# Kernel optimization log

Hardware: AMD Instinct MI355X
Metric: run time of the kernel (lower is better)

## Reference

```python
import jax, jax.numpy as jnp
import numpy as np

DIM, NH, HD = 1536, 12, 128
H, W, NFPB = 22, 40, 3
S = H * W * NFPB            # 2640 query tokens
PAST = 12 * H * W           # 10560 cached kv tokens
MAXF = 150                  # rope cache frames
EPS = 1e-6


def rmsnorm(y, g):
    # torch nn.RMSNorm over last dim
    return y * jax.lax.rsqrt(jnp.mean(y * y, axis=-1, keepdims=True) + EPS) * g


def build_rope_cache(freqs):
    # freqs: [MAXF, HD//2] angles -> flat (t,h,w) grid cache [MAXF*H*W, HD]
    hd2 = HD // 2               # 64
    c_h = hd2 // 3              # 21
    c_w = hd2 // 3              # 21
    c_t = hd2 - c_h - c_w       # 22
    f_t = freqs[:MAXF, :c_t]                       # [150, 22]
    f_h = freqs[:H, c_t:c_t + c_h]                 # [22, 21]
    f_w = freqs[:W, c_t + c_h:]                    # [40, 21]
    t_grid = jnp.broadcast_to(f_t[:, None, None, :], (MAXF, H, W, c_t))
    h_grid = jnp.broadcast_to(f_h[None, :, None, :], (MAXF, H, W, c_h))
    w_grid = jnp.broadcast_to(f_w[None, None, :, :], (MAXF, H, W, c_w))
    flat = jnp.concatenate([t_grid, h_grid, w_grid], -1).reshape(-1, hd2)
    return jnp.cos(flat), jnp.sin(flat)            # each [MAXF*H*W, 64]


def apply_rope_interleaved(t, cos, sin):
    # t: [s, n, HD]; cos/sin: [s, HD//2]; is_neox=False -> interleaved pairs
    te = t[..., 0::2]
    to = t[..., 1::2]
    c = cos[:, None, :]
    s = sin[:, None, :]
    oe = te * c - to * s
    oo = to * c + te * s
    return jnp.stack([oe, oo], axis=-1).reshape(t.shape)


def setup_inputs() -> dict:
    key = jax.random.key(0)
    ks = jax.random.split(key, 14)
    sc = 1.0 / np.sqrt(DIM)
    return {
        "x": jax.random.normal(ks[0], (1, S, DIM), jnp.float32),
        "freqs": jax.random.uniform(ks[1], (MAXF, HD // 2), jnp.float32),
        "cached_k": jax.random.normal(ks[2], (PAST, NH, HD), jnp.float32),
        "cached_v": jax.random.normal(ks[3], (PAST, NH, HD), jnp.float32),
        "Wq": jax.random.normal(ks[4], (DIM, DIM), jnp.float32) * sc,
        "bq": jax.random.normal(ks[5], (DIM,), jnp.float32) * 0.01,
        "Wk": jax.random.normal(ks[6], (DIM, DIM), jnp.float32) * sc,
        "bk": jax.random.normal(ks[7], (DIM,), jnp.float32) * 0.01,
        "Wv": jax.random.normal(ks[8], (DIM, DIM), jnp.float32) * sc,
        "bv": jax.random.normal(ks[9], (DIM,), jnp.float32) * 0.01,
        "Wo": jax.random.normal(ks[10], (DIM, DIM), jnp.float32) * sc,
        "bo": jax.random.normal(ks[11], (DIM,), jnp.float32) * 0.01,
        "gq": jnp.ones((DIM,), jnp.float32),
        "gk": jnp.ones((DIM,), jnp.float32),
        "current_start": PAST,
    }


def reference(x, freqs, cached_k, cached_v, Wq, bq, Wk, bk, Wv, bv, Wo, bo, gq, gk, current_start):
    xs = x[0]                                       # [S, DIM], B == 1
    q = rmsnorm(xs @ Wq.T + bq, gq).reshape(S, NH, HD)
    k = rmsnorm(xs @ Wk.T + bk, gk).reshape(S, NH, HD)
    v = (xs @ Wv.T + bv).reshape(S, NH, HD)

    cos_all, sin_all = build_rope_cache(freqs)
    pos = jnp.arange(S, dtype=jnp.int32) + current_start
    cos, sin = cos_all[pos], sin_all[pos]           # [S, 64]
    q = apply_rope_interleaved(q, cos, sin)
    k = apply_rope_interleaved(k, cos, sin)

    k_lin = jnp.concatenate([cached_k, k], axis=0)  # [KV, NH, HD]
    v_lin = jnp.concatenate([cached_v, v], axis=0)

    scale = 1.0 / np.sqrt(HD)
    scores = jnp.einsum("snd,knd->nsk", q, k_lin) * scale   # [NH, S, KV]
    probs = jax.nn.softmax(scores, axis=-1)
    out = jnp.einsum("nsk,knd->snd", probs, v_lin).reshape(S, DIM)
    return (out @ Wo.T + bo)[None]                  # [1, S, DIM]
```

## Files before the change

### kernel.cpp

```cpp
#include <hip/hip_runtime.h>

typedef unsigned short u16;
typedef short short8 __attribute__((ext_vector_type(8)));
typedef short short4b __attribute__((ext_vector_type(4)));
typedef float f32x4 __attribute__((ext_vector_type(4)));
typedef u16 us4 __attribute__((ext_vector_type(4)));

#define DIM   1536
#define NH    12
#define HD    128
#define SQ_   2640
#define SPAD  2688
#define PAST_ 10560
#define LTOT  13200
#define LPAD  13248

__device__ __forceinline__ u16 f2bf(float f){
  unsigned u = __builtin_bit_cast(unsigned, f);
  u += 0x7fffu + ((u >> 16) & 1u);
  return (u16)(u >> 16);
}
__device__ __forceinline__ float bf2f(u16 h){
  unsigned u = ((unsigned)h) << 16;
  return __builtin_bit_cast(float, u);
}
__device__ __forceinline__ void gload_lds16(const void* g, void* l){
  __builtin_amdgcn_global_load_lds(
      (const __attribute__((address_space(1))) void*)g,
      (__attribute__((address_space(3))) void*)l, 16, 0, 0);
}
__device__ __forceinline__ f32x4 mfma16(short4b a, short4b b, f32x4 c){
#if __has_builtin(__builtin_amdgcn_mfma_f32_16x16x16bf16_1k)
  return __builtin_amdgcn_mfma_f32_16x16x16bf16_1k(a, b, c, 0, 0, 0);
#else
  asm("v_mfma_f32_16x16x16_bf16 %0, %1, %2, %0" : "+v"(c) : "v"(a), "v"(b));
  return c;
#endif
}

__global__ void k_cvt(const float* __restrict__ s, u16* __restrict__ d, int n4){
  int i = blockIdx.x * 256 + threadIdx.x;
  if (i < n4){
    float4 f = ((const float4*)s)[i];
    us4 u; u[0]=f2bf(f.x); u[1]=f2bf(f.y); u[2]=f2bf(f.z); u[3]=f2bf(f.w);
    ((us4*)d)[i] = u;
  }
}

__global__ void k_prep_x(const float* __restrict__ x, u16* __restrict__ AB){
  int i = blockIdx.x * 256 + threadIdx.x;
  int e = i * 4;
  us4 u; u[0]=0; u[1]=0; u[2]=0; u[3]=0;
  if (e < SQ_*DIM){
    float4 f = ((const float4*)x)[i];
    u[0]=f2bf(f.x); u[1]=f2bf(f.y); u[2]=f2bf(f.z); u[3]=f2bf(f.w);
  }
  ((us4*)AB)[i] = u;
}

__global__ void k_prep_cache(const float* __restrict__ src, u16* __restrict__ dst, int n4){
  int i = blockIdx.x * 256 + threadIdx.x;
  if (i >= n4) return;
  int e = i * 4;
  if (e < PAST_*DIM){
    float4 f = ((const float4*)src)[i];
    us4 u; u[0]=f2bf(f.x); u[1]=f2bf(f.y); u[2]=f2bf(f.z); u[3]=f2bf(f.w);
    ((us4*)dst)[i] = u;
  } else {
    us4 u; u[0]=0; u[1]=0; u[2]=0; u[3]=0;
    ((us4*)dst)[i - PAST_*DIM/4 + LTOT*DIM/4] = u;
  }
}

__global__ void k_zero(u16* __restrict__ d, int n4){
  int i = blockIdx.x * 256 + threadIdx.x;
  if (i < n4){ us4 u; u[0]=0; u[1]=0; u[2]=0; u[3]=0; ((us4*)d)[i] = u; }
}

__global__ __launch_bounds__(256) void gemm_qkv(
  const u16* __restrict__ A,
  const u16* __restrict__ W0, const u16* __restrict__ W1, const u16* __restrict__ W2,
  const float* __restrict__ b0, const float* __restrict__ b1, const float* __restrict__ b2,
  u16* __restrict__ QL, u16* __restrict__ KL, u16* __restrict__ VA)
{
  __shared__ __align__(16) u16 As[4096];
  __shared__ __align__(16) u16 Bs[4096];
  int mt = blockIdx.x, nt = blockIdx.y;
  int tid = threadIdx.x, lane = tid & 63, w = tid >> 6;
  int wr = w >> 1, wc = w & 1;
  int which = nt / 12;
  const u16*  Bp = which==0 ? W0 : (which==1 ? W1 : W2);
  const float* bp = which==0 ? b0 : (which==1 ? b1 : b2);
  int nloc = (nt % 12) * 128;
  f32x4 acc[4][4];
  #pragma unroll
  for (int i=0;i<4;i++)
    #pragma unroll
    for (int j=0;j<4;j++) acc[i][j] = (f32x4){0.f,0.f,0.f,0.f};

  for (int k0 = 0; k0 < DIM; k0 += 32){
    #pragma unroll
    for (int p=0;p<2;p++){
      int e = (p*256 + tid) * 8;
      int r = e >> 5, c = e & 31;
      gload_lds16(A  + (size_t)(mt*128 + r)*DIM + k0 + c, (char*)As + p*4096 + (w<<10));
      gload_lds16(Bp + (size_t)(nloc   + r)*DIM + k0 + c, (char*)Bs + p*4096 + (w<<10));
    }
    __syncthreads();
    short8 af[4], bfr[4];
    #pragma unroll
    for (int i=0;i<4;i++){
      af[i]  = *(const short8*)&As[(wr*64 + i*16 + (lane&15))*32 + (lane>>4)*8];
      bfr[i] = *(const short8*)&Bs[(wc*64 + i*16 + (lane&15))*32 + (lane>>4)*8];
    }
    #pragma unroll
    for (int i=0;i<4;i++)
      #pragma unroll
      for (int j=0;j<4;j++)
        acc[i][j] = __builtin_amdgcn_mfma_f32_16x16x32_bf16(af[i], bfr[j], acc[i][j], 0,0,0);
    __syncthreads();
  }
  int rbase = mt*128 + wr*64;
  int cbase = nloc + wc*64;
  #pragma unroll
  for (int j=0;j<4;j++){
    int col = cbase + j*16 + (lane&15);
    float bb = bp[col];
    #pragma unroll
    for (int i=0;i<4;i++){
      #pragma unroll
      for (int q=0;q<4;q++){
        int row = rbase + i*16 + (lane>>4)*4 + q;
        if (row < SQ_){
          u16 uv = f2bf(acc[i][j][q] + bb);
          if (which==0)      QL[(size_t)row*DIM + col] = uv;
          else if (which==1) KL[(size_t)row*DIM + col] = uv;
          else               VA[(size_t)(PAST_ + row)*DIM + col] = uv;
        }
      }
    }
  }
}

__global__ __launch_bounds__(256) void gemm_out(
  const u16* __restrict__ A, const u16* __restrict__ W,
  const float* __restrict__ bias, float* __restrict__ out)
{
  __shared__ __align__(16) u16 As[4096];
  __shared__ __align__(16) u16 Bs[4096];
  int mt = blockIdx.x, nt = blockIdx.y;
  int tid = threadIdx.x, lane = tid & 63, w = tid >> 6;
  int wr = w >> 1, wc = w & 1;
  int nloc = nt * 128;
  f32x4 acc[4][4];
  #pragma unroll
  for (int i=0;i<4;i++)
    #pragma unroll
    for (int j=0;j<4;j++) acc[i][j] = (f32x4){0.f,0.f,0.f,0.f};

  for (int k0 = 0; k0 < DIM; k0 += 32){
    #pragma unroll
    for (int p=0;p<2;p++){
      int e = (p*256 + tid) * 8;
      int r = e >> 5, c = e & 31;
      gload_lds16(A + (size_t)(mt*128 + r)*DIM + k0 + c, (char*)As + p*4096 + (w<<10));
      gload_lds16(W + (size_t)(nloc   + r)*DIM + k0 + c, (char*)Bs + p*4096 + (w<<10));
    }
    __syncthreads();
    short8 af[4], bfr[4];
    #pragma unroll
    for (int i=0;i<4;i++){
      af[i]  = *(const short8*)&As[(wr*64 + i*16 + (lane&15))*32 + (lane>>4)*8];
      bfr[i] = *(const short8*)&Bs[(wc*64 + i*16 + (lane&15))*32 + (lane>>4)*8];
    }
    #pragma unroll
    for (int i=0;i<4;i++)
      #pragma unroll
      for (int j=0;j<4;j++)
        acc[i][j] = __builtin_amdgcn_mfma_f32_16x16x32_bf16(af[i], bfr[j], acc[i][j], 0,0,0);
    __syncthreads();
  }
  int rbase = mt*128 + wr*64;
  int cbase = nloc + wc*64;
  #pragma unroll
  for (int j=0;j<4;j++){
    int col = cbase + j*16 + (lane&15);
    float bb = bias[col];
    #pragma unroll
    for (int i=0;i<4;i++){
      #pragma unroll
      for (int q=0;q<4;q++){
        int row = rbase + i*16 + (lane>>4)*4 + q;
        if (row < SQ_) out[(size_t)row*DIM + col] = acc[i][j][q] + bb;
      }
    }
  }
}

__global__ __launch_bounds__(256) void norm_rope(
  const u16* __restrict__ QL, const u16* __restrict__ KL,
  const float* __restrict__ freqs, const float* __restrict__ gq, const float* __restrict__ gk,
  const int* __restrict__ cs,
  u16* __restrict__ Qout, u16* __restrict__ KAout)
{
  int s = blockIdx.x;
  int isk = blockIdx.y;
  int tid = threadIdx.x;
  const u16* src = (isk ? KL : QL) + (size_t)s*DIM + tid*6;
  float y[6];
  #pragma unroll
  for (int t=0;t<6;t++) y[t] = bf2f(src[t]);
  float ss = 0.f;
  #pragma unroll
  for (int t=0;t<6;t++) ss += y[t]*y[t];
  for (int mk=1; mk<64; mk<<=1) ss += __shfl_xor(ss, mk);
  __shared__ float red[4];
  if ((tid & 63) == 0) red[tid>>6] = ss;
  __syncthreads();
  float rn = rsqrtf((red[0]+red[1]+red[2]+red[3]) * (1.0f/1536.0f) + 1e-6f);
  rn *= isk ? 1.0f : 0.12752961954336302f;
  const float* g = (isk ? gk : gq) + tid*6;
  int pos = cs[0] + s;
  int tpos = pos / 880, rem = pos % 880;
  int hh = rem / 40, wp = rem % 40;
  u16 ov[6];
  #pragma unroll
  for (int pi=0; pi<3; pi++){
    int p = tid*3 + pi;
    int i = p & 63;
    int fr = (i < 22) ? tpos : ((i < 43) ? hh : wp);
    float ang = freqs[fr*64 + i];
    float sn, c;
    sincosf(ang, &sn, &c);
    float e  = y[pi*2]   * rn * g[pi*2];
    float od = y[pi*2+1] * rn * g[pi*2+1];
    ov[pi*2]   = f2bf(e*c - od*sn);
    ov[pi*2+1] = f2bf(od*c + e*sn);
  }
  u16* dst = isk ? (KAout + (size_t)(PAST_ + s)*DIM + tid*6)
                 : (Qout  + (size_t)s*DIM + tid*6);
  #pragma unroll
  for (int t=0;t<6;t++) dst[t] = ov[t];
}

__global__ __launch_bounds__(256, 2) void attn(
  const u16* __restrict__ Qf, const u16* __restrict__ KA,
  const u16* __restrict__ VA, u16* __restrict__ OP, float* __restrict__ ML)
{
  __shared__ __align__(16) u16 Ks[64*128];
  __shared__ __align__(16) u16 Vt[128*64];
  int h = blockIdx.y, qt = blockIdx.x, z = blockIdx.z;
  int tid = threadIdx.x, lane = tid & 63, w = tid >> 6;
  int g = lane >> 4, q = lane & 15;
  int qrow0 = qt*128 + w*32;
  int kvbeg = z ? 6656 : 0;
  int kvend = z ? LPAD : 6656;
  short8 qa[2][4];
  #pragma unroll
  for (int cq=0;cq<2;cq++){
    const u16* qb = Qf + (size_t)(qrow0 + cq*16 + q)*DIM + h*HD + g*8;
    #pragma unroll
    for (int kt=0;kt<4;kt++) qa[cq][kt] = *(const short8*)(qb + kt*32);
  }
  f32x4 o[2][8];
  #pragma unroll
  for (int cq=0;cq<2;cq++)
    #pragma unroll
    for (int dt=0;dt<8;dt++) o[cq][dt] = (f32x4){0.f,0.f,0.f,0.f};
  float m[2] = {-1e30f,-1e30f};
  float l[2] = {0.f,0.f};

  for (int kv0 = kvbeg; kv0 < kvend; kv0 += 64){
    #pragma unroll
    for (int p=0;p<4;p++){
      int e = w*2048 + p*512 + lane*8;
      int r = e >> 7;
      int bcol = (e & 127) << 1;
      int sb = bcol ^ ((r & 7) << 4);
      gload_lds16(KA + (size_t)(kv0 + r)*DIM + h*HD + (sb>>1),
                  (char*)Ks + w*4096 + p*1024);
    }
    {
      int c0 = (tid >> 4) << 3;
      int r0 = (tid & 15) << 2;
      const u16* vs = VA + (size_t)(kv0 + r0)*DIM + h*HD + c0;
      short8 v0 = *(const short8*)(vs);
      short8 v1 = *(const short8*)(vs + DIM);
      short8 v2 = *(const short8*)(vs + 2*DIM);
      short8 v3 = *(const short8*)(vs + 3*DIM);
      #pragma unroll
      for (int j=0;j<8;j++){
        int d = c0 + j;
        int key = ((d & 7) << 4) | (((d >> 3) & 1) << 3);
        int off = d*128 + ((r0*2) ^ key);
        us4 pk; pk[0]=(u16)v0[j]; pk[1]=(u16)v1[j]; pk[2]=(u16)v2[j]; pk[3]=(u16)v3[j];
        *(us4*)((char*)Vt + off) = pk;
      }
    }
    __syncthreads();
    f32x4 s4[2][4];
    #pragma unroll
    for (int cq=0;cq<2;cq++)
      #pragma unroll
      for (int ct=0;ct<4;ct++) s4[cq][ct] = (f32x4){0.f,0.f,0.f,0.f};
    #pragma unroll
    for (int ct=0;ct<4;ct++){
      int row = ct*16 + q;
      int rbyte = row*256, sw = (row & 7) << 4;
      #pragma unroll
      for (int kt=0;kt<4;kt++){
        int b = (kt*64 + (g<<4)) ^ sw;
        short8 kb = *(const short8*)((const char*)Ks + rbyte + b);
        s4[0][ct] = __builtin_amdgcn_mfma_f32_16x16x32_bf16(kb, qa[0][kt], s4[0][ct], 0,0,0);
        s4[1][ct] = __builtin_amdgcn_mfma_f32_16x16x32_bf16(kb, qa[1][kt], s4[1][ct], 0,0,0);
      }
    }
    if (kv0 + 64 > LTOT){
      #pragma unroll
      for (int ct=0;ct<4;ct++)
        #pragma unroll
        for (int j=0;j<4;j++)
          if (kv0 + ct*16 + g*4 + j >= LTOT){ s4[0][ct][j] = -1e30f; s4[1][ct][j] = -1e30f; }
    }
    float rm[2];
    #pragma unroll
    for (int cq=0;cq<2;cq++){
      float r_ = fmaxf(fmaxf(s4[cq][0][0],s4[cq][0][1]), fmaxf(s4[cq][0][2],s4[cq][0][3]));
      r_ = fmaxf(r_, fmaxf(fmaxf(s4[cq][1][0],s4[cq][1][1]), fmaxf(s4[cq][1][2],s4[cq][1][3])));
      r_ = fmaxf(r_, fmaxf(fmaxf(s4[cq][2][0],s4[cq][2][1]), fmaxf(s4[cq][2][2],s4[cq][2][3])));
      r_ = fmaxf(r_, fmaxf(fmaxf(s4[cq][3][0],s4[cq][3][1]), fmaxf(s4[cq][3][2],s4[cq][3][3])));
      r_ = fmaxf(r_, __shfl_xor(r_, 16));
      r_ = fmaxf(r_, __shfl_xor(r_, 32));
      rm[cq] = r_;
    }
    if (__any((rm[0] > m[0]+8.f) | (rm[1] > m[1]+8.f))){
      #pragma unroll
      for (int cq=0;cq<2;cq++){
        float mn = fmaxf(m[cq], rm[cq]);
        float al = exp2f(m[cq] - mn);
        m[cq] = mn;
        l[cq] *= al;
        #pragma unroll
        for (int dt=0;dt<8;dt++){
          f32x4 t = o[cq][dt];
          t[0]*=al; t[1]*=al; t[2]*=al; t[3]*=al;
          o[cq][dt] = t;
        }
      }
    }
    short4b pb[2][4];
    #pragma unroll
    for (int cq=0;cq<2;cq++){
      float rs = 0.f;
      #pragma unroll
      for (int ct=0;ct<4;ct++){
        short4b pk_;
        #pragma unroll
        for (int j=0;j<4;j++){
          float e2 = exp2f(s4[cq][ct][j] - m[cq]);
          rs += e2;
          pk_[j] = (short)f2bf(e2);
        }
        pb[cq][ct] = pk_;
      }
      rs += __shfl_xor(rs, 16);
      rs += __shfl_xor(rs, 32);
      l[cq] += rs;
    }
    #pragma unroll
    for (int dt=0;dt<8;dt++){
      int d = dt*16 + q;
      int key = ((d & 7) << 4) | (((d >> 3) & 1) << 3);
      int rbyte = d*128;
      #pragma unroll
      for (int ct=0;ct<4;ct++){
        int b = (ct*32 + (g<<3)) ^ key;
        short4b va_ = *(const short4b*)((const char*)Vt + rbyte + b);
        o[0][dt] = mfma16(va_, pb[0][ct], o[0][dt]);
        o[1][dt] = mfma16(va_, pb[1][ct], o[1][dt]);
      }
    }
    __syncthreads();
  }
  #pragma unroll
  for (int cq=0;cq<2;cq++){
    int row = qrow0 + cq*16 + q;
    size_t ob = ((size_t)(z*SPAD + row)*NH + h)*HD;
    #pragma unroll
    for (int dt=0;dt<8;dt++){
      us4 pk;
      #pragma unroll
      for (int j=0;j<4;j++) pk[j] = f2bf(o[cq][dt][j]);
      *(us4*)&OP[ob + dt*16 + g*4] = pk;
    }
    if (g == 0){
      size_t mb = ((size_t)(z*SPAD + row)*NH + h)*2;
      ML[mb] = m[cq]; ML[mb+1] = l[cq];
    }
  }
}

__global__ void merge_attn(const u16* __restrict__ OP, const float* __restrict__ ML,
                           u16* __restrict__ AB)
{
  int s = blockIdx.x, h = blockIdx.y, d = threadIdx.x;
  size_t i1 = ((size_t)s*NH + h)*2;
  size_t i2 = ((size_t)(SPAD + s)*NH + h)*2;
  float m1 = ML[i1], l1 = ML[i1+1];
  float m2 = ML[i2], l2 = ML[i2+1];
  float M = fmaxf(m1, m2);
  float e1 = exp2f(m1 - M), e2 = exp2f(m2 - M);
  float den = 1.0f / (l1*e1 + l2*e2);
  float o1 = bf2f(OP[((size_t)s*NH + h)*HD + d]);
  float o2 = bf2f(OP[((size_t)(SPAD + s)*NH + h)*HD + d]);
  AB[(size_t)s*DIM + h*HD + d] = f2bf((o1*e1 + o2*e2) * den);
}

extern "C" void kernel_launch(void* const* d_in, const int* in_sizes, int n_in,
                              void* d_out, int out_size, void* d_ws, size_t ws_size,
                              hipStream_t stream) {
  (void)in_sizes; (void)n_in; (void)out_size; (void)ws_size;
  const float* x    = (const float*)d_in[0];
  const float* freqs= (const float*)d_in[1];
  const float* ck   = (const float*)d_in[2];
  const float* cv   = (const float*)d_in[3];
  const float* Wq   = (const float*)d_in[4];
  const float* bq   = (const float*)d_in[5];
  const float* Wk   = (const float*)d_in[6];
  const float* bk   = (const float*)d_in[7];
  const float* Wv   = (const float*)d_in[8];
  const float* bv   = (const float*)d_in[9];
  const float* Wo   = (const float*)d_in[10];
  const float* bo   = (const float*)d_in[11];
  const float* gq   = (const float*)d_in[12];
  const float* gk   = (const float*)d_in[13];
  const int*   cs   = (const int*)d_in[14];
  float* out = (float*)d_out;
  char* ws = (char*)d_ws;

  u16* AB  = (u16*)(ws);
  u16* Wb3 = (u16*)(ws + 8257536);
  u16* QL  = (u16*)(ws + 12976128);
  u16* KA  = (u16*)(ws + 21233664);
  u16* VA  = (u16*)(ws + 61931520);
  u16* Wb0 = (u16*)(ws + 102629376);
  u16* Wb1 = (u16*)(ws + 107347968);
  u16* Wb2 = (u16*)(ws + 112066560);
  u16* KL  = (u16*)(ws + 116785152);
  u16*   OP = (u16*)(ws + 102629376);
  float* ML = (float*)(ws + 119144448);

  k_cvt<<<2304, 256, 0, stream>>>(Wq, Wb0, 589824);
  k_cvt<<<2304, 256, 0, stream>>>(Wk, Wb1, 589824);
  k_cvt<<<2304, 256, 0, stream>>>(Wv, Wb2, 589824);
  k_cvt<<<2304, 256, 0, stream>>>(Wo, Wb3, 589824);
  k_prep_x<<<4032, 256, 0, stream>>>(x, AB);
  k_prep_cache<<<15912, 256, 0, stream>>>(ck, KA, 4073472);
  k_prep_cache<<<15912, 256, 0, stream>>>(cv, VA, 4073472);
  k_zero<<<72, 256, 0, stream>>>(QL + (size_t)SQ_*DIM, 18432);

  gemm_qkv<<<dim3(21,36), 256, 0, stream>>>(AB, Wb0, Wb1, Wb2, bq, bk, bv, QL, KL, VA);
  norm_rope<<<dim3(2640,2), 256, 0, stream>>>(QL, KL, freqs, gq, gk, cs, QL, KA);
  attn<<<dim3(21,12,2), 256, 0, stream>>>(QL, KA, VA, OP, ML);
  merge_attn<<<dim3(2640,12), 128, 0, stream>>>(OP, ML, AB);
  gemm_out<<<dim3(21,12), 256, 0, stream>>>(AB, Wb3, bo, out);
}
```

Before: 569.2 us.

## Double-buffer K/V LDS tiles in attention and use packed bf16 conversion

The attention kernel now keeps two LDS buffers for K and transposed V. While the current tile is computed, it issues the next tile's async K loads and V register loads, and it writes the transposed V after the PV step. This drops one barrier per iteration and hides global load latency. It also replaces the software bf16 rounding with the hardware v_cvt_pk_bf16_f32 instruction and rebalances the max-reduction tree. LDS use doubles to 64KB per block, which may limit occupancy under launch_bounds(256,2), and the prefetched V registers add register pressure.

```diff
diff --git a/kernel.cpp b/kernel.cpp
--- a/kernel.cpp
+++ b/kernel.cpp
@@ -5,6 +5,7 @@
 typedef short short4b __attribute__((ext_vector_type(4)));
 typedef float f32x4 __attribute__((ext_vector_type(4)));
 typedef u16 us4 __attribute__((ext_vector_type(4)));
+typedef unsigned u32x2 __attribute__((ext_vector_type(2)));
 
 #define DIM   1536
 #define NH    12
@@ -23,6 +24,11 @@
 __device__ __forceinline__ float bf2f(u16 h){
   unsigned u = ((unsigned)h) << 16;
   return __builtin_bit_cast(float, u);
+}
+__device__ __forceinline__ unsigned cvtpk_bf16(float lo, float hi){
+  unsigned r;
+  asm("v_cvt_pk_bf16_f32 %0, %1, %2" : "=v"(r) : "v"(lo), "v"(hi));
+  return r;
 }
 __device__ __forceinline__ void gload_lds16(const void* g, void* l){
   __builtin_amdgcn_global_load_lds(
@@ -247,14 +253,17 @@
   const u16* __restrict__ Qf, const u16* __restrict__ KA,
   const u16* __restrict__ VA, u16* __restrict__ OP, float* __restrict__ ML)
 {
-  __shared__ __align__(16) u16 Ks[64*128];
-  __shared__ __align__(16) u16 Vt[128*64];
+  __shared__ __align__(16) u16 Ks[2][64*128];
+  __shared__ __align__(16) u16 Vt[2][128*64];
   int h = blockIdx.y, qt = blockIdx.x, z = blockIdx.z;
   int tid = threadIdx.x, lane = tid & 63, w = tid >> 6;
   int g = lane >> 4, q = lane & 15;
   int qrow0 = qt*128 + w*32;
   int kvbeg = z ? 6656 : 0;
   int kvend = z ? LPAD : 6656;
+  int c0 = (tid >> 4) << 3;
+  int r0 = (tid & 15) << 2;
+
   short8 qa[2][4];
   #pragma unroll
   for (int cq=0;cq<2;cq++){
@@ -270,7 +279,7 @@
   float m[2] = {-1e30f,-1e30f};
   float l[2] = {0.f,0.f};
 
-  for (int kv0 = kvbeg; kv0 < kvend; kv0 += 64){
+  auto stageK = [&](int kv0, u16* dK){
     #pragma unroll
     for (int p=0;p<4;p++){
       int e = w*2048 + p*512 + lane*8;
@@ -278,31 +287,47 @@
       int bcol = (e & 127) << 1;
       int sb = bcol ^ ((r & 7) << 4);
       gload_lds16(KA + (size_t)(kv0 + r)*DIM + h*HD + (sb>>1),
-                  (char*)Ks + w*4096 + p*1024);
-    }
-    {
-      int c0 = (tid >> 4) << 3;
-      int r0 = (tid & 15) << 2;
-      const u16* vs = VA + (size_t)(kv0 + r0)*DIM + h*HD + c0;
-      short8 v0 = *(const short8*)(vs);
-      short8 v1 = *(const short8*)(vs + DIM);
-      short8 v2 = *(const short8*)(vs + 2*DIM);
-      short8 v3 = *(const short8*)(vs + 3*DIM);
-      #pragma unroll
-      for (int j=0;j<8;j++){
-        int d = c0 + j;
-        int key = ((d & 7) << 4) | (((d >> 3) & 1) << 3);
-        int off = d*128 + ((r0*2) ^ key);
-        us4 pk; pk[0]=(u16)v0[j]; pk[1]=(u16)v1[j]; pk[2]=(u16)v2[j]; pk[3]=(u16)v3[j];
-        *(us4*)((char*)Vt + off) = pk;
-      }
-    }
-    __syncthreads();
+                  (char*)dK + w*4096 + p*1024);
+    }
+  };
+  auto loadV = [&](int kv0, short8* vr){
+    const u16* vs = VA + (size_t)(kv0 + r0)*DIM + h*HD + c0;
+    vr[0] = *(const short8*)(vs);
+    vr[1] = *(const short8*)(vs + DIM);
+    vr[2] = *(const short8*)(vs + 2*DIM);
+    vr[3] = *(const short8*)(vs + 3*DIM);
+  };
+  auto writeVt = [&](u16* dV, short8* vr){
+    #pragma unroll
+    for (int j=0;j<8;j++){
+      int d = c0 + j;
+      int key = ((d & 7) << 4) | (((d >> 3) & 1) << 3);
+      int off = d*128 + ((r0*2) ^ key);
+      us4 pk; pk[0]=(u16)vr[0][j]; pk[1]=(u16)vr[1][j]; pk[2]=(u16)vr[2][j]; pk[3]=(u16)vr[3][j];
+      *(us4*)((char*)dV + off) = pk;
+    }
+  };
+
+  short8 vr[4];
+  int cur = 0;
+  stageK(kvbeg, &Ks[0][0]);
+  loadV(kvbeg, vr);
+  writeVt(&Vt[0][0], vr);
+  __syncthreads();
+
+  for (int kv0 = kvbeg; kv0 < kvend; kv0 += 64){
+    int nxt = kv0 + 64;
+    bool has_next = nxt < kvend;
+    if (has_next){
+      stageK(nxt, &Ks[cur^1][0]);
+      loadV(nxt, vr);
+    }
     f32x4 s4[2][4];
     #pragma unroll
     for (int cq=0;cq<2;cq++)
       #pragma unroll
       for (int ct=0;ct<4;ct++) s4[cq][ct] = (f32x4){0.f,0.f,0.f,0.f};
+    const u16* ksb = &Ks[cur][0];
     #pragma unroll
     for (int ct=0;ct<4;ct++){
       int row = ct*16 + q;
@@ -310,7 +335,7 @@
       #pragma unroll
       for (int kt=0;kt<4;kt++){
         int b = (kt*64 + (g<<4)) ^ sw;
-        short8 kb = *(const short8*)((const char*)Ks + rbyte + b);
+        short8 kb = *(const short8*)((const char*)ksb + rbyte + b);
         s4[0][ct] = __builtin_amdgcn_mfma_f32_16x16x32_bf16(kb, qa[0][kt], s4[0][ct], 0,0,0);
         s4[1][ct] = __builtin_amdgcn_mfma_f32_16x16x32_bf16(kb, qa[1][kt], s4[1][ct], 0,0,0);
       }
@@ -325,10 +350,12 @@
     float rm[2];
     #pragma unroll
     for (int cq=0;cq<2;cq++){
-      float r_ = fmaxf(fmaxf(s4[cq][0][0],s4[cq][0][1]), fmaxf(s4[cq][0][2],s4[cq][0][3]));
-      r_ = fmaxf(r_, fmaxf(fmaxf(s4[cq][1][0],s4[cq][1][1]), fmaxf(s4[cq][1][2],s4[cq][1][3])));
-      r_ = fmaxf(r_, fmaxf(fmaxf(s4[cq][2][0],s4[cq][2][1]), fmaxf(s4[cq][2][2],s4[cq][2][3])));
-      r_ = fmaxf(r_, fmaxf(fmaxf(s4[cq][3][0],s4[cq][3][1]), fmaxf(s4[cq][3][2],s4[cq][3][3])));
+      float a0 = fmaxf(fmaxf(s4[cq][0][0], s4[cq][0][1]), s4[cq][0][2]);
+      float a1 = fmaxf(fmaxf(s4[cq][0][3], s4[cq][1][0]), s4[cq][1][1]);
+      float a2 = fmaxf(fmaxf(s4[cq][1][2], s4[cq][1][3]), s4[cq][2][0]);
+      float a3 = fmaxf(fmaxf(s4[cq][2][1], s4[cq][2][2]), s4[cq][2][3]);
+      float a4 = fmaxf(fmaxf(s4[cq][3][0], s4[cq][3][1]), s4[cq][3][2]);
+      float r_ = fmaxf(fmaxf(a0, a1), fmaxf(fmaxf(a2, a3), fmaxf(a4, s4[cq][3][3])));
       r_ = fmaxf(r_, __shfl_xor(r_, 16));
       r_ = fmaxf(r_, __shfl_xor(r_, 32));
       rm[cq] = r_;
@@ -354,19 +381,19 @@
       float rs = 0.f;
       #pragma unroll
       for (int ct=0;ct<4;ct++){
-        short4b pk_;
-        #pragma unroll
-        for (int j=0;j<4;j++){
-          float e2 = exp2f(s4[cq][ct][j] - m[cq]);
-          rs += e2;
-          pk_[j] = (short)f2bf(e2);
-        }
-        pb[cq][ct] = pk_;
+        float e0 = exp2f(s4[cq][ct][0] - m[cq]);
+        float e1 = exp2f(s4[cq][ct][1] - m[cq]);
+        float e2 = exp2f(s4[cq][ct][2] - m[cq]);
+        float e3 = exp2f(s4[cq][ct][3] - m[cq]);
+        rs += (e0 + e1) + (e2 + e3);
+        u32x2 pw = { cvtpk_bf16(e0, e1), cvtpk_bf16(e2, e3) };
+        pb[cq][ct] = __builtin_bit_cast(short4b, pw);
       }
       rs += __shfl_xor(rs, 16);
       rs += __shfl_xor(rs, 32);
       l[cq] += rs;
     }
+    const u16* vtb = &Vt[cur][0];
     #pragma unroll
     for (int dt=0;dt<8;dt++){
       int d = dt*16 + q;
@@ -375,12 +402,16 @@
       #pragma unroll
       for (int ct=0;ct<4;ct++){
         int b = (ct*32 + (g<<3)) ^ key;
-        short4b va_ = *(const short4b*)((const char*)Vt + rbyte + b);
+        short4b va_ = *(const short4b*)((const char*)vtb + rbyte + b);
         o[0][dt] = mfma16(va_, pb[0][ct], o[0][dt]);
         o[1][dt] = mfma16(va_, pb[1][ct], o[1][dt]);
       }
     }
-    __syncthreads();
+    if (has_next){
+      writeVt(&Vt[cur^1][0], vr);
+      __syncthreads();
+      cur ^= 1;
+    }
   }
   #pragma unroll
   for (int cq=0;cq<2;cq++){
@@ -388,10 +419,9 @@
     size_t ob = ((size_t)(z*SPAD + row)*NH + h)*HD;
     #pragma unroll
     for (int dt=0;dt<8;dt++){
-      us4 pk;
-      #pragma unroll
-      for (int j=0;j<4;j++) pk[j] = f2bf(o[cq][dt][j]);
-      *(us4*)&OP[ob + dt*16 + g*4] = pk;
+      u32x2 pw = { cvtpk_bf16(o[cq][dt][0], o[cq][dt][1]),
+                   cvtpk_bf16(o[cq][dt][2], o[cq][dt][3]) };
+      *(u32x2*)&OP[ob + dt*16 + g*4] = pw;
     }
     if (g == 0){
       size_t mb = ((size_t)(z*SPAD + row)*NH + h)*2;
```

Measured after the change: 533.4 us. -6.3%, faster.
